# Kernel optimization log

Hardware: AMD Instinct MI355X
Metric: run time of the kernel (lower is better)

The kernel has to match this reference:

```python
import jax, jax.numpy as jnp
import numpy as np


def _conv1x1(x, w, b):
    # x: [B,C,H,W], w: [Cout,Cin], b: [Cout]  (1x1 conv == per-pixel linear)
    return jnp.einsum('bchw,oc->bohw', x, w) + b[None, :, None, None]


def setup_inputs() -> dict:
    key = jax.random.key(0)
    ks = jax.random.split(key, 8)
    B, C, H, W = 8, 128, 128, 128
    s = 1.0 / np.sqrt(C)
    return {
        'q_feat': jax.random.normal(ks[0], (B, C, H, W), jnp.float32),
        'kv_feat': jax.random.normal(ks[1], (B, C, H, W), jnp.float32),
        'q_w': jax.random.normal(ks[2], (C, C), jnp.float32) * s,
        'q_b': jax.random.normal(ks[3], (C,), jnp.float32) * 0.01,
        'k_w': jax.random.normal(ks[4], (C, C), jnp.float32) * s,
        'k_b': jax.random.normal(ks[5], (C,), jnp.float32) * 0.01,
        'v_w': jax.random.normal(ks[6], (C, C), jnp.float32) * s,
        'v_b': jax.random.normal(ks[7], (C,), jnp.float32) * 0.01,
    }


def reference(q_feat, kv_feat, q_w, q_b, k_w, k_b, v_w, v_b):
    B, C, H, W = q_feat.shape
    q = _conv1x1(q_feat, q_w, q_b).reshape(B, C, H * W)   # [B,C,N]
    k = _conv1x1(kv_feat, k_w, k_b).reshape(B, C, H * W)  # [B,C,N]
    v = _conv1x1(kv_feat, v_w, v_b).reshape(B, C, H * W)  # [B,C,N]
    k_sm = jax.nn.softmax(k, axis=-1)                     # softmax over spatial dim N
    context = jnp.einsum('bcn,bdn->bcd', v, k_sm)         # [B,C,C]
    out = jnp.einsum('bcd,bdn->bcn', context, q)          # [B,C,N]
    return out.reshape(B, C, H, W)
```

## Files before the change

### kernel.cpp

```cpp
#include <hip/hip_runtime.h>
#include <hip/hip_bf16.h>
#include <cstdint>

#define B_ 8
#define C_ 128
#define N_ 16384
#define CHN 512
#define SN 128
#define NST 4
#define NC (N_ / CHN)

typedef __attribute__((ext_vector_type(8))) short short8;
typedef __attribute__((ext_vector_type(4))) float f32x4;
typedef __attribute__((ext_vector_type(4))) unsigned short us4;
typedef unsigned short u16;

__device__ __forceinline__ short f2bf(float f) {
  union { float f; unsigned u; } c; c.f = f;
  unsigned r = (c.u + 0x7FFFu + ((c.u >> 16) & 1u)) >> 16;
  return (short)r;
}

__device__ __forceinline__ unsigned cvtpk(float lo, float hi) {
  unsigned r;
  asm("v_cvt_pk_bf16_f32 %0, %1, %2" : "=v"(r) : "v"(lo), "v"(hi));
  return r;
}

union SB { short8 s8; unsigned u[4]; };

__global__ __launch_bounds__(256) void k0_wcvt(const float* __restrict__ kw,
                                               const float* __restrict__ vw,
                                               u16* __restrict__ wbf) {
  const int g = blockIdx.x * 256 + threadIdx.x;
  const int mat = g >> 12, o4 = g & 4095;
  const float* src = mat ? vw : kw;
  float4 f = reinterpret_cast<const float4*>(src)[o4];
  us4 s;
  s[0] = (u16)f2bf(f.x); s[1] = (u16)f2bf(f.y);
  s[2] = (u16)f2bf(f.z); s[3] = (u16)f2bf(f.w);
  reinterpret_cast<us4*>(wbf + (size_t)mat * C_ * C_)[o4] = s;
}

#define KA_LOADS(ST_) do {                                                   \
  _Pragma("unroll") for (int h_ = 0; h_ < 2; ++h_)                           \
  _Pragma("unroll") for (int j_ = 0; j_ < 16; ++j_)                          \
    xr[h_][j_] = xw[(size_t)j_ * N_ + (ST_) * SN + h_ * 64 + lane];          \
} while (0)

#define KA_XWRITE(BUF_) do {                                                 \
  _Pragma("unroll") for (int h_ = 0; h_ < 2; ++h_) {                         \
    const int n_ = h_ * 64 + lane;                                           \
    unsigned pk_[8];                                                         \
    _Pragma("unroll") for (int p_ = 0; p_ < 8; ++p_)                         \
      pk_[p_] = cvtpk(xr[h_][2 * p_], xr[h_][2 * p_ + 1]);                   \
    _Pragma("unroll") for (int o_ = 0; o_ < 2; ++o_) {                       \
      uint4 q_;                                                              \
      q_.x = pk_[o_ * 4]; q_.y = pk_[o_ * 4 + 1];                            \
      q_.z = pk_[o_ * 4 + 2]; q_.w = pk_[o_ * 4 + 3];                        \
      *reinterpret_cast<uint4*>(                                             \
          (BUF_) + n_ * SN + ((w * 16 + o_ * 8) ^ ((n_ & 7) << 3))) = q_;    \
    }                                                                        \
  }                                                                          \
} while (0)

__global__ __launch_bounds__(512, 2) void ka_projctx(
    const float* __restrict__ kv, const u16* __restrict__ wbf,
    const float* __restrict__ kb, const float* __restrict__ vb,
    float* __restrict__ part, float* __restrict__ zpart) {
  __shared__ u16 xt[2][C_ * SN];
  __shared__ u16 eks[C_ * SN];
  __shared__ u16 vs [C_ * SN];

  const int fid = blockIdx.x + blockIdx.y * NC;
  const int fid2 = (fid & 7) * 32 + (fid >> 3);
  const int b = fid2 >> 5, kc = fid2 & 31;
  const int tid = threadIdx.x;
  const int w = tid >> 6, lane = tid & 63;
  const int lg = lane >> 4, li = lane & 15;
  const int mat = w >> 2, dblk = w & 3;
  const int cg = w >> 1, dh = w & 1;

  const float* xb = kv + (size_t)b * C_ * N_ + (size_t)kc * CHN;
  const float* xw = xb + (size_t)(w * 16) * N_;
  const u16* Wm = wbf + (size_t)mat * C_ * C_;
  const float* biasp = mat ? vb : kb;
  u16* S = mat ? vs : eks;

  short8 wreg[2][4];
#pragma unroll
  for (int dt = 0; dt < 2; ++dt)
#pragma unroll
    for (int ks = 0; ks < 4; ++ks)
      wreg[dt][ks] = *reinterpret_cast<const short8*>(
          Wm + (dblk * 32 + dt * 16 + li) * C_ + ks * 32 + lg * 8);
  float bias2[2];
#pragma unroll
  for (int dt = 0; dt < 2; ++dt) bias2[dt] = biasp[dblk * 32 + dt * 16 + li];

  f32x4 acc[2][4] = {};
  float zac[2] = {0.f, 0.f};
  float xr[2][16];

  KA_LOADS(0);
  KA_XWRITE(&xt[0][0]);
  KA_LOADS(1);
  asm volatile("s_waitcnt lgkmcnt(0)" ::: "memory");
  __builtin_amdgcn_s_barrier();
  __builtin_amdgcn_sched_barrier(0);

#pragma unroll
  for (int st = 0; st < NST; ++st) {
    const u16* xc = &xt[st & 1][0];

    if (st < NST - 1) {
      KA_XWRITE(&xt[(st + 1) & 1][0]);
      if (st < NST - 2) KA_LOADS(st + 2);
    }

#pragma unroll
    for (int h2 = 0; h2 < 4; ++h2) {
      f32x4 pacc[2][2] = {};
#pragma unroll
      for (int ntl = 0; ntl < 2; ++ntl) {
        const int n = (h2 * 2 + ntl) * 16 + li;
#pragma unroll
        for (int ks = 0; ks < 4; ++ks) {
          short8 a = *reinterpret_cast<const short8*>(
              xc + n * SN + ((ks * 32 + lg * 8) ^ ((n & 7) << 3)));
#pragma unroll
          for (int dt = 0; dt < 2; ++dt)
            pacc[ntl][dt] = __builtin_amdgcn_mfma_f32_16x16x32_bf16(
                a, wreg[dt][ks], pacc[ntl][dt], 0, 0, 0);
        }
      }
#pragma unroll
      for (int dt = 0; dt < 2; ++dt) {
        const int d = dblk * 32 + dt * 16 + li;
        const float bias = bias2[dt];
#pragma unroll
        for (int ntl = 0; ntl < 2; ++ntl) {
          float v0 = pacc[ntl][dt][0] + bias;
          float v1 = pacc[ntl][dt][1] + bias;
          float v2 = pacc[ntl][dt][2] + bias;
          float v3 = pacc[ntl][dt][3] + bias;
          if (mat == 0) {
            v0 = __expf(v0); v1 = __expf(v1); v2 = __expf(v2); v3 = __expf(v3);
            zac[dt] += (v0 + v1) + (v2 + v3);
          }
          const int nq = (h2 * 2 + ntl) * 16 + lg * 4;
          uint2 pk; pk.x = cvtpk(v0, v1); pk.y = cvtpk(v2, v3);
          *reinterpret_cast<uint2*>(S + d * SN + (nq ^ ((d & 7) << 3))) = pk;
        }
      }
    }
    asm volatile("s_waitcnt lgkmcnt(0)" ::: "memory");
    __builtin_amdgcn_s_barrier();
    __builtin_amdgcn_sched_barrier(0);

#pragma unroll
    for (int kk = 0; kk < 4; ++kk) {
      const int n0 = kk * 32 + lg * 8;
      short8 a[2], bb[4];
#pragma unroll
      for (int am = 0; am < 2; ++am) {
        const int c = cg * 32 + am * 16 + li;
        a[am] = *reinterpret_cast<const short8*>(vs + c * SN + (n0 ^ ((c & 7) << 3)));
      }
#pragma unroll
      for (int dt = 0; dt < 4; ++dt) {
        const int d = dh * 64 + dt * 16 + li;
        bb[dt] = *reinterpret_cast<const short8*>(eks + d * SN + (n0 ^ ((d & 7) << 3)));
      }
#pragma unroll
      for (int am = 0; am < 2; ++am)
#pragma unroll
        for (int dt = 0; dt < 4; ++dt)
          acc[am][dt] = __builtin_amdgcn_mfma_f32_16x16x32_bf16(a[am], bb[dt], acc[am][dt], 0, 0, 0);
    }
    asm volatile("s_waitcnt lgkmcnt(0)" ::: "memory");
    __builtin_amdgcn_s_barrier();
    __builtin_amdgcn_sched_barrier(0);
  }

  float* P = part + ((size_t)kc * B_ + b) * C_ * C_;
#pragma unroll
  for (int am = 0; am < 2; ++am)
#pragma unroll
    for (int dt = 0; dt < 4; ++dt)
#pragma unroll
      for (int r = 0; r < 4; ++r) {
        const int c = cg * 32 + am * 16 + lg * 4 + r;
        const int d = dh * 64 + dt * 16 + li;
        P[c * C_ + d] = acc[am][dt][r];
      }
  if (mat == 0) {
#pragma unroll
    for (int dt = 0; dt < 2; ++dt) {
      float z = zac[dt];
      z += __shfl_xor(z, 16);
      z += __shfl_xor(z, 32);
      if (lg == 0)
        zpart[((size_t)kc * B_ + b) * C_ + dblk * 32 + dt * 16 + li] = z;
    }
  }
}

__global__ __launch_bounds__(256) void kb2_fin(
    const float* __restrict__ part, const float* __restrict__ zpart,
    const float* __restrict__ qw, const float* __restrict__ qb,
    u16* __restrict__ M, float* __restrict__ T) {
  const int b = blockIdx.y;
  const int cs0 = blockIdx.x * 16;
  const int tid = threadIdx.x;
  __shared__ float cs[16][128];
  __shared__ float Zs[128];
  if (tid < 128) {
    float s = 0.f;
    for (int kc = 0; kc < NC; ++kc)
      s += zpart[((size_t)kc * B_ + b) * C_ + tid];
    Zs[tid] = s;
  }
  __syncthreads();
#pragma unroll
  for (int i = 0; i < 8; ++i) {
    const int e = tid + i * 256;
    const int cl = e >> 7, d = e & 127;
    float s = 0.f;
    for (int kc = 0; kc < NC; ++kc)
      s += part[(((size_t)kc * B_ + b) * C_ + (cs0 + cl)) * C_ + d];
    cs[cl][d] = s / Zs[d];
  }
  __syncthreads();
  const int cl = tid >> 4, e0 = (tid & 15) * 8;
  float m[8] = {};
  for (int d = 0; d < 128; ++d) {
    const float cv = cs[cl][d];
    const float* qr = qw + d * C_ + e0;
#pragma unroll
    for (int j = 0; j < 8; ++j) m[j] += cv * qr[j];
  }
  u16* mp = M + ((size_t)b * C_ + cs0 + cl) * C_ + e0;
#pragma unroll
  for (int j = 0; j < 8; ++j) mp[j] = (u16)f2bf(m[j]);
  if (tid < 16) {
    float tv = 0.f;
    for (int d = 0; d < 128; ++d) tv += cs[tid][d] * qb[d];
    T[b * C_ + cs0 + tid] = tv;
  }
}

#define K4_LOADS(ST_) do {                                                   \
  _Pragma("unroll") for (int h_ = 0; h_ < 2; ++h_)                           \
  _Pragma("unroll") for (int j_ = 0; j_ < 16; ++j_)                          \
    xr[h_][j_] = qw_[(size_t)j_ * N_ + (ST_) * SN + h_ * 64 + lane];         \
} while (0)

#define K4_XWRITE(BUF_) do {                                                 \
  _Pragma("unroll") for (int h_ = 0; h_ < 2; ++h_) {                         \
    const int n_ = h_ * 64 + lane;                                           \
    unsigned pk_[8];                                                         \
    _Pragma("unroll") for (int p_ = 0; p_ < 8; ++p_)                         \
      pk_[p_] = cvtpk(xr[h_][2 * p_], xr[h_][2 * p_ + 1]);                   \
    _Pragma("unroll") for (int o_ = 0; o_ < 2; ++o_) {                       \
      uint4 q_;                                                              \
      q_.x = pk_[o_ * 4]; q_.y = pk_[o_ * 4 + 1];                            \
      q_.z = pk_[o_ * 4 + 2]; q_.w = pk_[o_ * 4 + 3];                        \
      *reinterpret_cast<uint4*>(                                             \
          (BUF_) + n_ * SN + ((w * 16 + o_ * 8) ^ ((n_ & 7) << 3))) = q_;    \
    }                                                                        \
  }                                                                          \
} while (0)

__global__ __launch_bounds__(512) void k4_out(const u16* __restrict__ M,
                                              const float* __restrict__ T,
                                              const float* __restrict__ q,
                                              float* __restrict__ out) {
  __shared__ u16 qt[2][SN * C_];

  const int fid = blockIdx.x + blockIdx.y * NC;
  const int fid2 = (fid & 7) * 32 + (fid >> 3);
  const int b = fid2 >> 5, kc = fid2 & 31;
  const int nb = kc * CHN;
  const int tid = threadIdx.x;
  const int w = tid >> 6, lane = tid & 63;
  const int lg = lane >> 4, li = lane & 15;

  const float* qw_ = q + (size_t)b * C_ * N_ + nb + (size_t)(w * 16) * N_;

  short8 mreg[4];
  const u16* Mb = M + (size_t)b * C_ * C_;
#pragma unroll
  for (int ks = 0; ks < 4; ++ks)
    mreg[ks] = *reinterpret_cast<const short8*>(
        Mb + (w * 16 + li) * C_ + ks * 32 + lg * 8);
  float tcv[4];
#pragma unroll
  for (int r = 0; r < 4; ++r) tcv[r] = T[b * C_ + w * 16 + lg * 4 + r];

  float xr[2][16];

  K4_LOADS(0);
  K4_XWRITE(&qt[0][0]);
  K4_LOADS(1);
  asm volatile("s_waitcnt lgkmcnt(0)" ::: "memory");
  __builtin_amdgcn_s_barrier();
  __builtin_amdgcn_sched_barrier(0);

#pragma unroll
  for (int st = 0; st < NST; ++st) {
    const u16* xc = &qt[st & 1][0];

    if (st < NST - 1) {
      K4_XWRITE(&qt[(st + 1) & 1][0]);
      if (st < NST - 2) K4_LOADS(st + 2);
    }

    f32x4 acc[8] = {};
#pragma unroll
    for (int nt = 0; nt < 8; ++nt) {
      const int n = nt * 16 + li;
#pragma unroll
      for (int ks = 0; ks < 4; ++ks) {
        short8 bb = *reinterpret_cast<const short8*>(
            xc + n * SN + ((ks * 32 + lg * 8) ^ ((n & 7) << 3)));
        acc[nt] = __builtin_amdgcn_mfma_f32_16x16x32_bf16(
            mreg[ks], bb, acc[nt], 0, 0, 0);
      }
    }

#pragma unroll
    for (int r = 0; r < 4; ++r) {
      const int c = w * 16 + lg * 4 + r;
      float* op = out + ((size_t)b * C_ + c) * N_ + nb + st * SN;
      const float t = tcv[r];
#pragma unroll
      for (int nt = 0; nt < 8; ++nt)
        op[nt * 16 + li] = acc[nt][r] + t;
    }

    asm volatile("s_waitcnt lgkmcnt(0)" ::: "memory");
    __builtin_amdgcn_s_barrier();
    __builtin_amdgcn_sched_barrier(0);
  }
}

extern "C" void kernel_launch(void* const* d_in, const int* in_sizes, int n_in,
                              void* d_out, int out_size, void* d_ws, size_t ws_size,
                              hipStream_t stream) {
  const float* q_feat  = (const float*)d_in[0];
  const float* kv_feat = (const float*)d_in[1];
  const float* q_w = (const float*)d_in[2];
  const float* q_b = (const float*)d_in[3];
  const float* k_w = (const float*)d_in[4];
  const float* k_b = (const float*)d_in[5];
  const float* v_w = (const float*)d_in[6];
  const float* v_b = (const float*)d_in[7];
  float* out = (float*)d_out;

  char* ws = (char*)d_ws;
  const size_t szPart = (size_t)NC * B_ * C_ * C_ * sizeof(float);
  const size_t szZp   = (size_t)NC * B_ * C_ * sizeof(float);
  const size_t szWbf  = (size_t)2 * C_ * C_ * sizeof(u16);
  const size_t szM    = (size_t)B_ * C_ * C_ * sizeof(u16);

  float* part  = (float*)ws;
  float* zpart = (float*)(ws + szPart);
  u16*   wbf   = (u16*)(ws + szPart + szZp);
  u16*   M     = (u16*)(ws + szPart + szZp + szWbf);
  float* T     = (float*)(ws + szPart + szZp + szWbf + szM);

  k0_wcvt<<<dim3(32), 256, 0, stream>>>(k_w, v_w, wbf);
  ka_projctx<<<dim3(NC, B_), 512, 0, stream>>>(kv_feat, wbf, k_b, v_b, part, zpart);
  kb2_fin<<<dim3(8, B_), 256, 0, stream>>>(part, zpart, q_w, q_b, M, T);
  k4_out<<<dim3(NC, B_), 512, 0, stream>>>(M, T, q_feat, out);
}
```

Measured before the change: 73.22 us.

## Split output kernel by output-channel group over long N slabs

Reassigns k4_out work: each of 256 blocks now handles one batch, a 16-output-channel group and a 4096-wide N slab, looping over 32 double-buffered stages instead of 4. Each wave computes a 16x16 tile per stage with a single row of M held in registers. The aim is a different schedule and store pattern for the output, but every block still stages all 128 input channels of q. As a result, q is read from global memory and converted to bf16 eight times redundantly. Each stage also does far fewer MFMAs per barrier.

```diff
diff --git a/kernel.cpp b/kernel.cpp
--- a/kernel.cpp
+++ b/kernel.cpp
@@ -253,7 +253,7 @@
 #define K4_LOADS(ST_) do {                                                   \
   _Pragma("unroll") for (int h_ = 0; h_ < 2; ++h_)                           \
   _Pragma("unroll") for (int j_ = 0; j_ < 16; ++j_)                          \
-    xr[h_][j_] = qw_[(size_t)j_ * N_ + (ST_) * SN + h_ * 64 + lane];         \
+    xr[h_][j_] = qsrc[(size_t)j_ * N_ + (ST_) * SN + h_ * 64 + lane];        \
 } while (0)
 
 #define K4_XWRITE(BUF_) do {                                                 \
@@ -272,76 +272,79 @@
   }                                                                          \
 } while (0)
 
+#define K4_BODY(CUR_, ST_) do {                                              \
+  f32x4 acc = {};                                                            \
+  const int n_ = w * 16 + li;                                                \
+  _Pragma("unroll") for (int ks_ = 0; ks_ < 4; ++ks_) {                      \
+    short8 bb_ = *reinterpret_cast<const short8*>(                           \
+        (CUR_) + n_ * SN + ((ks_ * 32 + lg * 8) ^ ((n_ & 7) << 3)));         \
+    acc = __builtin_amdgcn_mfma_f32_16x16x32_bf16(mreg[ks_], bb_, acc, 0, 0, 0); \
+  }                                                                          \
+  _Pragma("unroll") for (int r_ = 0; r_ < 4; ++r_) {                         \
+    const int c_ = cgrp * 16 + lg * 4 + r_;                                  \
+    out[((size_t)b * C_ + c_) * N_ + nbase + (ST_) * SN + w * 16 + li] =     \
+        acc[r_] + tcv[r_];                                                   \
+  }                                                                          \
+} while (0)
+
 __global__ __launch_bounds__(512) void k4_out(const u16* __restrict__ M,
                                               const float* __restrict__ T,
                                               const float* __restrict__ q,
                                               float* __restrict__ out) {
-  __shared__ u16 qt[2][SN * C_];
-
-  const int fid = blockIdx.x + blockIdx.y * NC;
-  const int fid2 = (fid & 7) * 32 + (fid >> 3);
-  const int b = fid2 >> 5, kc = fid2 & 31;
-  const int nb = kc * CHN;
+  __shared__ u16 qt0[SN * C_];
+  __shared__ u16 qt1[SN * C_];
+
+  const int bid = blockIdx.x;
+  const int b = bid & 7;
+  const int j = bid >> 3;
+  const int cgrp = j & 7;
+  const int nslab = j >> 3;
+  const int nbase = nslab * 4096;
   const int tid = threadIdx.x;
   const int w = tid >> 6, lane = tid & 63;
   const int lg = lane >> 4, li = lane & 15;
 
-  const float* qw_ = q + (size_t)b * C_ * N_ + nb + (size_t)(w * 16) * N_;
+  const float* qsrc = q + (size_t)b * C_ * N_ + nbase + (size_t)(w * 16) * N_;
 
   short8 mreg[4];
   const u16* Mb = M + (size_t)b * C_ * C_;
 #pragma unroll
   for (int ks = 0; ks < 4; ++ks)
     mreg[ks] = *reinterpret_cast<const short8*>(
-        Mb + (w * 16 + li) * C_ + ks * 32 + lg * 8);
+        Mb + (cgrp * 16 + li) * C_ + ks * 32 + lg * 8);
   float tcv[4];
 #pragma unroll
-  for (int r = 0; r < 4; ++r) tcv[r] = T[b * C_ + w * 16 + lg * 4 + r];
+  for (int r = 0; r < 4; ++r) tcv[r] = T[b * C_ + cgrp * 16 + lg * 4 + r];
 
   float xr[2][16];
 
   K4_LOADS(0);
-  K4_XWRITE(&qt[0][0]);
+  K4_XWRITE(qt0);
   K4_LOADS(1);
   asm volatile("s_waitcnt lgkmcnt(0)" ::: "memory");
   __builtin_amdgcn_s_barrier();
   __builtin_amdgcn_sched_barrier(0);
 
-#pragma unroll
-  for (int st = 0; st < NST; ++st) {
-    const u16* xc = &qt[st & 1][0];
-
-    if (st < NST - 1) {
-      K4_XWRITE(&qt[(st + 1) & 1][0]);
-      if (st < NST - 2) K4_LOADS(st + 2);
-    }
-
-    f32x4 acc[8] = {};
-#pragma unroll
-    for (int nt = 0; nt < 8; ++nt) {
-      const int n = nt * 16 + li;
-#pragma unroll
-      for (int ks = 0; ks < 4; ++ks) {
-        short8 bb = *reinterpret_cast<const short8*>(
-            xc + n * SN + ((ks * 32 + lg * 8) ^ ((n & 7) << 3)));
-        acc[nt] = __builtin_amdgcn_mfma_f32_16x16x32_bf16(
-            mreg[ks], bb, acc[nt], 0, 0, 0);
-      }
-    }
-
-#pragma unroll
-    for (int r = 0; r < 4; ++r) {
-      const int c = w * 16 + lg * 4 + r;
-      float* op = out + ((size_t)b * C_ + c) * N_ + nb + st * SN;
-      const float t = tcv[r];
-#pragma unroll
-      for (int nt = 0; nt < 8; ++nt)
-        op[nt * 16 + li] = acc[nt][r] + t;
-    }
-
-    asm volatile("s_waitcnt lgkmcnt(0)" ::: "memory");
-    __builtin_amdgcn_s_barrier();
-    __builtin_amdgcn_sched_barrier(0);
+  for (int st2 = 0; st2 < 16; ++st2) {
+    const int st = st2 * 2;
+    {
+      K4_XWRITE(qt1);
+      if (st < 30) K4_LOADS(st + 2);
+      K4_BODY(qt0, st);
+      asm volatile("s_waitcnt lgkmcnt(0)" ::: "memory");
+      __builtin_amdgcn_s_barrier();
+      __builtin_amdgcn_sched_barrier(0);
+    }
+    {
+      if (st < 30) {
+        K4_XWRITE(qt0);
+        if (st < 29) K4_LOADS(st + 3);
+      }
+      K4_BODY(qt1, st + 1);
+      asm volatile("s_waitcnt lgkmcnt(0)" ::: "memory");
+      __builtin_amdgcn_s_barrier();
+      __builtin_amdgcn_sched_barrier(0);
+    }
   }
 }
 
@@ -373,5 +376,5 @@
   k0_wcvt<<<dim3(32), 256, 0, stream>>>(k_w, v_w, wbf);
   ka_projctx<<<dim3(NC, B_), 512, 0, stream>>>(kv_feat, wbf, k_b, v_b, part, zpart);
   kb2_fin<<<dim3(8, B_), 256, 0, stream>>>(part, zpart, q_w, q_b, M, T);
-  k4_out<<<dim3(NC, B_), 512, 0, stream>>>(M, T, q_feat, out);
-}
+  k4_out<<<dim3(256), 512, 0, stream>>>(M, T, q_feat, out);
+}
```

Result: slower. 87.73 us (+19.8%).
